# Kernel optimization log

Hardware: AMD Instinct MI355X
Metric: run time of the kernel (lower is better)

The kernel has to match this reference:

```python
import jax, jax.numpy as jnp
import numpy as np

B, T, C = 2, 2048, 2048
H, HD = 16, 128          # n_head, head_dim
DC, DC1 = 672, 672        # kv / q compression dims
DR = 64                   # decoupled rope dim
DN = HD - DR              # nope dim = 64
GATE_CH = 32


def _rope(x, cos, sin):
    # x: (B,T,h,D); cos/sin: (B,T,D//2) -> broadcast over heads
    cos = cos[:, :, None, :]
    sin = sin[:, :, None, :]
    d = x.shape[-1] // 2
    x1, x2 = x[..., :d], x[..., d:]
    return jnp.concatenate([x1 * cos + x2 * sin, -x1 * sin + x2 * cos], axis=-1)


def _rmsnorm(x):
    eps = jnp.finfo(x.dtype).eps
    return x * jax.lax.rsqrt(jnp.mean(jnp.square(x), axis=-1, keepdims=True) + eps)


def setup_inputs() -> dict:
    key = jax.random.key(0)
    ks = jax.random.split(key, 10)
    x = jax.random.normal(ks[0], (B, T, C), jnp.float32)
    ve = jax.random.normal(ks[1], (B, T, H * HD), jnp.float32)
    # rotary tables for d_rope//2 = 32 frequencies
    inv_freq = 1.0 / (10000.0 ** (jnp.arange(DR // 2, dtype=jnp.float32) / (DR // 2)))
    ang = jnp.arange(T, dtype=jnp.float32)[:, None] * inv_freq[None, :]  # (T, DR//2)
    cos = jnp.broadcast_to(jnp.cos(ang)[None], (B, T, DR // 2)).astype(jnp.float32)
    sin = jnp.broadcast_to(jnp.sin(ang)[None], (B, T, DR // 2)).astype(jnp.float32)
    s = 0.02
    w_dkv = s * jax.random.normal(ks[2], (C, DC), jnp.float32)
    w_ukv = s * jax.random.normal(ks[3], (DC, H * (DN + HD)), jnp.float32)
    w_kr = s * jax.random.normal(ks[4], (C, DR), jnp.float32)
    w_dq = s * jax.random.normal(ks[5], (C, DC1), jnp.float32)
    w_q = s * jax.random.normal(ks[6], (DC1, H * HD), jnp.float32)
    w_cproj = s * jax.random.normal(ks[7], (H * HD, C), jnp.float32)
    w_ve_gate = s * jax.random.normal(ks[8], (GATE_CH, H), jnp.float32)
    return {"x": x, "ve": ve, "cos": cos, "sin": sin,
            "w_dkv": w_dkv, "w_ukv": w_ukv, "w_kr": w_kr, "w_dq": w_dq,
            "w_q": w_q, "w_cproj": w_cproj, "w_ve_gate": w_ve_gate,
            "window_size": 0}


def reference(x, ve, cos, sin, w_dkv, w_ukv, w_kr, w_dq, w_q, w_cproj, w_ve_gate, window_size):
    b, t, _ = x.shape
    # low-rank KV path
    c_kv = x @ w_dkv                                   # (B,T,DC)
    kv = (c_kv @ w_ukv).reshape(b, t, H, DN + HD)
    k_nope, v = kv[..., :DN], kv[..., DN:]
    # decoupled rope key (single shared head)
    k_rope = (x @ w_kr).reshape(b, t, 1, DR)
    k_rope = _rope(k_rope, cos, sin)
    # value-embedding gate
    gate = 2.0 * jax.nn.sigmoid(x[..., :GATE_CH] @ w_ve_gate)   # (B,T,H)
    v = v + gate[..., None] * ve.reshape(b, t, H, HD)
    # low-rank Q path
    q = ((x @ w_dq) @ w_q).reshape(b, t, H, HD)
    q_nope, q_rope = q[..., :DN], q[..., DN:]
    q_rope = _rope(q_rope, cos, sin)
    k = jnp.concatenate([k_nope, jnp.broadcast_to(k_rope, (b, t, H, DR))], axis=-1)
    q = jnp.concatenate([q_nope, q_rope], axis=-1)
    q, k = _rmsnorm(q), _rmsnorm(k)
    # causal attention (window_size==0 -> full causal, matching window_size=(-1,-1))
    scale = 1.0 / jnp.sqrt(jnp.float32(HD))
    scores = jnp.einsum('bqhd,bkhd->bhqk', q, k) * scale
    causal = jnp.tril(jnp.ones((t, t), dtype=bool))
    scores = jnp.where(causal[None, None], scores, jnp.finfo(scores.dtype).min)
    att = jax.nn.softmax(scores, axis=-1)
    y = jnp.einsum('bhqk,bkhd->bqhd', att, v).reshape(b, t, H * HD)
    return y @ w_cproj
```

## Files before the change

### kernel.cpp

```cpp
#include <hip/hip_runtime.h>
#include <hip/hip_bf16.h>

typedef unsigned short u16;
typedef unsigned int u32;
typedef __bf16 bf16x8 __attribute__((ext_vector_type(8)));
typedef float f32x4 __attribute__((ext_vector_type(4)));
typedef u16 ushort8 __attribute__((ext_vector_type(8)));

#define TSEQ 2048
#define NHEAD 16

#define GLD16(gp, lp) __builtin_amdgcn_global_load_lds( \
    (__attribute__((address_space(1))) void*)(gp), \
    (__attribute__((address_space(3))) void*)(lp), 16, 0, 0)

static __device__ __forceinline__ float bf2f(u16 u) {
  unsigned int x = ((unsigned int)u) << 16;
  union { unsigned int i; float f; } c; c.i = x; return c.f;
}
static __device__ __forceinline__ u16 f2bf(float f) {
  union { float f; unsigned int i; } c; c.f = f;
  unsigned int x = c.i;
  unsigned int r = (x + 0x7FFFu + ((x >> 16) & 1u)) >> 16;
  return (u16)r;
}
static __device__ __forceinline__ void st_out(u16* p, float v) { *p = f2bf(v); }
static __device__ __forceinline__ void st_out(float* p, float v) { *p = v; }
static __device__ __forceinline__ u32 cvtpk(float lo, float hi) {
  u32 w;
  asm("v_cvt_pk_bf16_f32 %0, %1, %2" : "=v"(w) : "v"(lo), "v"(hi));
  return w;
}

__global__ __launch_bounds__(256) void k_conv_x(const float* __restrict__ x, u16* __restrict__ xb) {
  size_t i = ((size_t)blockIdx.x * 256 + threadIdx.x) * 8;
  float4 a = *(const float4*)(x + i);
  float4 b = *(const float4*)(x + i + 4);
  ushort8 o;
  o[0] = f2bf(a.x); o[1] = f2bf(a.y); o[2] = f2bf(a.z); o[3] = f2bf(a.w);
  o[4] = f2bf(b.x); o[5] = f2bf(b.y); o[6] = f2bf(b.z); o[7] = f2bf(b.w);
  *(ushort8*)(xb + i) = o;
}

__global__ __launch_bounds__(256) void k_tconv(const float* __restrict__ src, u16* __restrict__ dst,
                                               int R, int Cc, int Rpad) {
  __shared__ float sm[32][33];
  int tx = threadIdx.x & 31, ty = threadIdx.x >> 5;
  int r0 = blockIdx.x * 32, c0 = blockIdx.y * 32;
#pragma unroll
  for (int i = 0; i < 4; i++) {
    int r = r0 + ty + 8 * i;
    int c = c0 + tx;
    sm[ty + 8 * i][tx] = (r < R && c < Cc) ? src[(size_t)r * Cc + c] : 0.f;
  }
  __syncthreads();
#pragma unroll
  for (int i = 0; i < 4; i++) {
    int c = c0 + ty + 8 * i;
    dst[(size_t)c * Rpad + r0 + tx] = f2bf(sm[tx][ty + 8 * i]);
  }
}

__global__ __launch_bounds__(256) void k_gate(const float* __restrict__ x, const float* __restrict__ wg,
                                              float* __restrict__ gate) {
  int idx = blockIdx.x * 256 + threadIdx.x;
  int m = idx >> 4, h = idx & 15;
  const float* xr = x + (size_t)m * 2048;
  float s = 0.f;
#pragma unroll
  for (int j = 0; j < 32; j++) s += xr[j] * wg[j * 16 + h];
  gate[idx] = 2.f / (1.f + __expf(-s));
}

template <typename OT>
__global__ __launch_bounds__(256) void k_gemm128(const u16* __restrict__ A, int lda,
                                                 const u16* __restrict__ BT, int ldb,
                                                 OT* __restrict__ C, int ldc,
                                                 int K) {
  __shared__ __align__(16) u16 As[128 * 32];
  __shared__ __align__(16) u16 Bs[128 * 32];
  int t = threadIdx.x;
  int wid = t >> 6, lane = t & 63;
  int m0 = blockIdx.y * 128, n0 = blockIdx.x * 128;
  int c0 = wid * 2;
  int srow0 = c0 * 16 + (lane >> 2);
  int scol = (lane & 3) * 8;
  const u16* Ag0 = A + (size_t)(m0 + srow0) * lda + scol;
  const u16* Ag1 = A + (size_t)(m0 + srow0 + 16) * lda + scol;
  const u16* Bg0 = BT + (size_t)(n0 + srow0) * ldb + scol;
  const u16* Bg1 = BT + (size_t)(n0 + srow0 + 16) * ldb + scol;
  u16* Al0 = &As[c0 * 512];
  u16* Al1 = &As[c0 * 512 + 512];
  u16* Bl0 = &Bs[c0 * 512];
  u16* Bl1 = &Bs[c0 * 512 + 512];
  int wr = (wid >> 1) * 64, wc = (wid & 1) * 64;
  int fr = lane & 15, fo = (lane >> 4) * 8;
  f32x4 acc[4][4];
#pragma unroll
  for (int m = 0; m < 4; m++)
#pragma unroll
    for (int n = 0; n < 4; n++) acc[m][n] = (f32x4){0, 0, 0, 0};
  for (int k0 = 0; k0 < K; k0 += 32) {
    GLD16(Ag0 + k0, Al0);
    GLD16(Ag1 + k0, Al1);
    GLD16(Bg0 + k0, Bl0);
    GLD16(Bg1 + k0, Bl1);
    __syncthreads();
    bf16x8 af[4], bf[4];
#pragma unroll
    for (int m = 0; m < 4; m++) af[m] = *(const bf16x8*)&As[(wr + m * 16 + fr) * 32 + fo];
#pragma unroll
    for (int n = 0; n < 4; n++) bf[n] = *(const bf16x8*)&Bs[(wc + n * 16 + fr) * 32 + fo];
#pragma unroll
    for (int m = 0; m < 4; m++)
#pragma unroll
      for (int n = 0; n < 4; n++)
        acc[m][n] = __builtin_amdgcn_mfma_f32_16x16x32_bf16(af[m], bf[n], acc[m][n], 0, 0, 0);
    __syncthreads();
  }
  int cr = (lane >> 4) * 4, cc = lane & 15;
#pragma unroll
  for (int m = 0; m < 4; m++)
#pragma unroll
    for (int n = 0; n < 4; n++)
#pragma unroll
      for (int r = 0; r < 4; r++)
        st_out(&C[(size_t)(m0 + wr + m * 16 + cr + r) * ldc + n0 + wc + n * 16 + cc], acc[m][n][r]);
}

__global__ __launch_bounds__(256) void k_gemm_dual(const u16* __restrict__ catout,
                                                   const u16* __restrict__ wukvT,
                                                   u16* __restrict__ kvb,
                                                   const u16* __restrict__ wqT,
                                                   const float* __restrict__ cosp,
                                                   const float* __restrict__ sinp,
                                                   u16* __restrict__ qf) {
  __shared__ __align__(16) u16 As[128 * 32];
  __shared__ __align__(16) u16 Bs[128 * 32];
  int t = threadIdx.x;
  int wid = t >> 6, lane = t & 63;
  int bx = blockIdx.x;
  bool isq = (bx >= 24);
  int nx = isq ? bx - 24 : bx;
  int m0 = blockIdx.y * 128, n0 = nx * 128;
  const u16* A = isq ? catout + 768 : catout;
  const u16* BT = isq ? wqT : wukvT;
  int c0 = wid * 2;
  int srow0 = c0 * 16 + (lane >> 2);
  int scol = (lane & 3) * 8;
  const u16* Ag0 = A + (size_t)(m0 + srow0) * 1664 + scol;
  const u16* Ag1 = A + (size_t)(m0 + srow0 + 16) * 1664 + scol;
  const u16* Bg0 = BT + (size_t)(n0 + srow0) * 768 + scol;
  const u16* Bg1 = BT + (size_t)(n0 + srow0 + 16) * 768 + scol;
  u16* Al0 = &As[c0 * 512];
  u16* Al1 = &As[c0 * 512 + 512];
  u16* Bl0 = &Bs[c0 * 512];
  u16* Bl1 = &Bs[c0 * 512 + 512];
  int wr = (wid >> 1) * 64, wc = (wid & 1) * 64;
  int fr = lane & 15, fo = (lane >> 4) * 8;
  f32x4 acc[4][4];
#pragma unroll
  for (int m = 0; m < 4; m++)
#pragma unroll
    for (int n = 0; n < 4; n++) acc[m][n] = (f32x4){0, 0, 0, 0};
  for (int k0 = 0; k0 < 768; k0 += 32) {
    GLD16(Ag0 + k0, Al0);
    GLD16(Ag1 + k0, Al1);
    GLD16(Bg0 + k0, Bl0);
    GLD16(Bg1 + k0, Bl1);
    __syncthreads();
    bf16x8 af[4], bf[4];
#pragma unroll
    for (int m = 0; m < 4; m++) af[m] = *(const bf16x8*)&As[(wr + m * 16 + fr) * 32 + fo];
#pragma unroll
    for (int n = 0; n < 4; n++) bf[n] = *(const bf16x8*)&Bs[(wc + n * 16 + fr) * 32 + fo];
#pragma unroll
    for (int m = 0; m < 4; m++)
#pragma unroll
      for (int n = 0; n < 4; n++)
        acc[m][n] = __builtin_amdgcn_mfma_f32_16x16x32_bf16(af[m], bf[n], acc[m][n], 0, 0, 0);
    __syncthreads();
  }
  int cr = (lane >> 4) * 4, cc = lane & 15;
  if (!isq) {
#pragma unroll
    for (int m = 0; m < 4; m++)
#pragma unroll
      for (int n = 0; n < 4; n++)
#pragma unroll
        for (int r = 0; r < 4; r++)
          kvb[(size_t)(m0 + wr + m * 16 + cr + r) * 3072 + n0 + wc + n * 16 + cc] = f2bf(acc[m][n][r]);
    return;
  }
  int h = nx;
  int wch = wid & 1;
  int wrg = wid >> 1;
  if (wch == 1) {
#pragma unroll
    for (int m = 0; m < 4; m++)
#pragma unroll
      for (int r = 0; r < 4; r++) {
        int grow = m0 + wr + m * 16 + cr + r;
#pragma unroll
        for (int n = 0; n < 2; n++) {
          int i = n * 16 + cc;
          float cth = cosp[(size_t)grow * 32 + i];
          float sth = sinp[(size_t)grow * 32 + i];
          float x1 = acc[m][n][r], x2 = acc[m][n + 2][r];
          acc[m][n][r]     = x1 * cth + x2 * sth;
          acc[m][n + 2][r] = x2 * cth - x1 * sth;
        }
      }
  }
  float part[4][4];
#pragma unroll
  for (int m = 0; m < 4; m++)
#pragma unroll
    for (int r = 0; r < 4; r++) {
      float s2 = 0.f;
#pragma unroll
      for (int n = 0; n < 4; n++) s2 += acc[m][n][r] * acc[m][n][r];
#pragma unroll
      for (int o = 1; o < 16; o <<= 1) s2 += __shfl_xor(s2, o, 64);
      part[m][r] = s2;
    }
  float* xs = (float*)As;
  if (cc == 0) {
#pragma unroll
    for (int m = 0; m < 4; m++)
#pragma unroll
      for (int r = 0; r < 4; r++)
        xs[(wrg * 2 + wch) * 64 + m * 16 + cr + r] = part[m][r];
  }
  __syncthreads();
#pragma unroll
  for (int m = 0; m < 4; m++)
#pragma unroll
    for (int r = 0; r < 4; r++) {
      int lrow = m * 16 + cr + r;
      float tot = part[m][r] + xs[(wrg * 2 + (wch ^ 1)) * 64 + lrow];
      float rms = rsqrtf(tot * (1.f / 128.f) + 1.1920929e-7f) * 0.1275174245f;
      int grow = m0 + wr + lrow;
      int b2 = grow >> 11, tt = grow & 2047;
      size_t base = (((size_t)(b2 * NHEAD + h)) * TSEQ + tt) * 128 + wch * 64;
#pragma unroll
      for (int n = 0; n < 4; n++)
        qf[base + n * 16 + cc] = f2bf(acc[m][n][r] * rms);
    }
}

__global__ __launch_bounds__(256) void k_build_k(const u16* __restrict__ kv, const u16* __restrict__ kr,
                                                 const float* __restrict__ cosp, const float* __restrict__ sinp,
                                                 u16* __restrict__ ksw) {
  __shared__ __align__(16) u16 sm[8192];
  int tid = threadIdx.x, wid = tid >> 6, lane = tid & 63;
  int bh = blockIdx.x >> 5, tile = blockIdx.x & 31;
  int b = bh >> 4, h = bh & 15;
  int d0 = lane * 2;
  for (int rr = 0; rr < 16; rr++) {
    int row = wid * 16 + rr;
    int t = tile * 64 + row;
    int m = b * TSEQ + t;
    float v[2];
#pragma unroll
    for (int e = 0; e < 2; e++) {
      int d = d0 + e;
      float val;
      if (d < 64) {
        val = bf2f(kv[(size_t)m * 3072 + h * 192 + d]);
      } else {
        int dd = d - 64, i = dd & 31;
        float c = cosp[m * 32 + i], s = sinp[m * 32 + i];
        float x1 = bf2f(kr[(size_t)m * 1664 + i]), x2 = bf2f(kr[(size_t)m * 1664 + 32 + i]);
        val = (dd < 32) ? (x1 * c + x2 * s) : (x2 * c - x1 * s);
      }
      v[e] = val;
    }
    float ss = v[0] * v[0] + v[1] * v[1];
#pragma unroll
    for (int o = 1; o < 64; o <<= 1) ss += __shfl_xor(ss, o, 64);
    float rms = rsqrtf(ss * (1.f / 128.f) + 1.1920929e-7f);
    int a = (row * 256 + d0 * 2) ^ ((row & 7) << 4);
    sm[a >> 1] = f2bf(v[0] * rms);
    sm[(a >> 1) + 1] = f2bf(v[1] * rms);
  }
  __syncthreads();
  u16* dst = ksw + ((size_t)(bh * 32 + tile)) * 8192 + tid * 32;
  const u16* src = sm + tid * 32;
#pragma unroll
  for (int j = 0; j < 4; j++)
    *(ushort8*)(dst + j * 8) = *(const ushort8*)(src + j * 8);
}

__global__ __launch_bounds__(256) void k_build_v(const u16* __restrict__ kv, const float* __restrict__ ve,
                                                 const float* __restrict__ gate, u16* __restrict__ vsw) {
  __shared__ __align__(16) char sm[128 * 128];
  int bh = blockIdx.x >> 5, tile = blockIdx.x & 31;
  int t0 = tile * 64;
  int b = bh >> 4, h = bh & 15;
  int tt = threadIdx.x >> 2, dp = (threadIdx.x & 3) * 32;
  int m = b * TSEQ + t0 + tt;
  float g = gate[m * 16 + h];
  const u16* kvp = kv + (size_t)m * 3072 + h * 192 + 64 + dp;
  const float* vep = ve + (size_t)m * 2048 + h * 128 + dp;
  ushort8 kvv[4];
  float4 vev[8];
#pragma unroll
  for (int u = 0; u < 4; u++) kvv[u] = *(const ushort8*)(kvp + u * 8);
#pragma unroll
  for (int u = 0; u < 8; u++) vev[u] = *(const float4*)(vep + u * 4);
#pragma unroll
  for (int j = 0; j < 32; j++) {
    float vvf = ((const float*)&vev[j >> 2])[j & 3];
    float v = bf2f(kvv[j >> 3][j & 7]) + g * vvf;
    int row = dp + j;
    int a = row * 128 + tt * 2;
    *(u16*)(sm + (a ^ ((row & 7) << 4))) = f2bf(v);
  }
  __syncthreads();
  u16* dst = vsw + ((size_t)(bh * 32 + tile)) * 8192 + threadIdx.x * 32;
  const u16* src = (const u16*)sm + threadIdx.x * 32;
#pragma unroll
  for (int j = 0; j < 4; j++)
    *(ushort8*)(dst + j * 8) = *(const ushort8*)(src + j * 8);
}

__global__ __launch_bounds__(256, 2) void k_attn(const u16* __restrict__ qf, const u16* __restrict__ ksw,
                                                 const u16* __restrict__ vsw, u16* __restrict__ y) {
  __shared__ __align__(16) u16 kvbuf[2][2][8192];
  __shared__ __align__(16) char plds_all[4][4096];
  int tid = threadIdx.x, wid = tid >> 6, lane = tid & 63;
  int gq = lane >> 4, c = lane & 15;
  int task = (blockIdx.x & 7) * 64 + (blockIdx.x >> 3);
  int bh = task >> 4;
  int tq = task & 15;
  int qb = ((task >> 5) & 1) ? tq : 15 - tq;
  int nt = 2 * qb + 2;
  int q0w = qb * 128 + wid * 32;
  const u16* qp = qf + (size_t)bh * TSEQ * 128;
  const u16* kswb = ksw + (size_t)bh * 32 * 8192;
  const u16* vswb = vsw + (size_t)bh * 32 * 8192;
  char* plds = plds_all[wid];
  int swz = (c & 7) << 4;
  bf16x8 qfr[2][4];
#pragma unroll
  for (int rg = 0; rg < 2; rg++)
#pragma unroll
    for (int kc = 0; kc < 4; kc++)
      qfr[rg][kc] = *(const bf16x8*)(qp + (size_t)(q0w + rg * 16 + c) * 128 + kc * 32 + gq * 8);
  f32x4 oacc[2][8];
#pragma unroll
  for (int rg = 0; rg < 2; rg++)
#pragma unroll
    for (int nd = 0; nd < 8; nd++) oacc[rg][nd] = (f32x4){0, 0, 0, 0};
  float mreg[2] = {-1e30f, -1e30f}, lreg[2] = {0.f, 0.f};
  int chunk = wid * 4;
#pragma unroll
  for (int j = 0; j < 4; j++) {
    GLD16(kswb + (chunk + j) * 512 + lane * 8, &kvbuf[0][0][(chunk + j) * 512]);
    GLD16(vswb + (chunk + j) * 512 + lane * 8, &kvbuf[0][1][(chunk + j) * 512]);
  }
  __syncthreads();
  for (int it = 0; it < nt; it++) {
    int cur = it & 1;
    if (it + 1 < nt) {
      const u16* kt = kswb + (size_t)(it + 1) * 8192;
      const u16* vt = vswb + (size_t)(it + 1) * 8192;
#pragma unroll
      for (int j = 0; j < 4; j++) {
        GLD16(kt + (chunk + j) * 512 + lane * 8, &kvbuf[cur ^ 1][0][(chunk + j) * 512]);
        GLD16(vt + (chunk + j) * 512 + lane * 8, &kvbuf[cur ^ 1][1][(chunk + j) * 512]);
      }
    }
    int kt0 = it * 64;
    if (kt0 <= q0w + 31) {
      const char* Kt = (const char*)kvbuf[cur][0];
      const char* Vt = (const char*)kvbuf[cur][1];
      bool maskit = (kt0 + 63 > q0w);
      f32x4 sacc[2][4];
#pragma unroll
      for (int rg = 0; rg < 2; rg++)
#pragma unroll
        for (int s = 0; s < 4; s++) sacc[rg][s] = (f32x4){0, 0, 0, 0};
#pragma unroll
      for (int s = 0; s < 4; s++) {
        int row = s * 16 + c;
#pragma unroll
        for (int kc = 0; kc < 4; kc++) {
          int a = (row * 256 + (kc * 32 + gq * 8) * 2) ^ ((row & 7) << 4);
          bf16x8 kfr = *(const bf16x8*)(Kt + a);
          sacc[0][s] = __builtin_amdgcn_mfma_f32_16x16x32_bf16(kfr, qfr[0][kc], sacc[0][s], 0, 0, 0);
          sacc[1][s] = __builtin_amdgcn_mfma_f32_16x16x32_bf16(kfr, qfr[1][kc], sacc[1][s], 0, 0, 0);
        }
      }
      if (maskit) {
#pragma unroll
        for (int rg = 0; rg < 2; rg++) {
          int qrow = q0w + rg * 16 + c;
#pragma unroll
          for (int s = 0; s < 4; s++)
#pragma unroll
            for (int r = 0; r < 4; r++) {
              int key = kt0 + s * 16 + gq * 4 + r;
              sacc[rg][s][r] = (key <= qrow) ? sacc[rg][s][r] : -3e38f;
            }
        }
      }
      float mx[2];
#pragma unroll
      for (int rg = 0; rg < 2; rg++) {
        float m2 = sacc[rg][0][0];
#pragma unroll
        for (int s = 0; s < 4; s++)
#pragma unroll
          for (int r = 0; r < 4; r++) m2 = fmaxf(m2, sacc[rg][s][r]);
        m2 = fmaxf(m2, __shfl_xor(m2, 16, 64));
        m2 = fmaxf(m2, __shfl_xor(m2, 32, 64));
        mx[rg] = m2;
      }
      bool ok = (mx[0] - mreg[0] <= 11.f) && (mx[1] - mreg[1] <= 11.f);
      if (!__all(ok)) {
#pragma unroll
        for (int rg = 0; rg < 2; rg++) {
          float mn = fmaxf(mreg[rg], mx[rg]);
          float fac = exp2f(mreg[rg] - mn);
          lreg[rg] *= fac;
          float fq[4];
#pragma unroll
          for (int r = 0; r < 4; r++) fq[r] = __shfl(fac, gq * 4 + r, 64);
#pragma unroll
          for (int nd = 0; nd < 8; nd++)
#pragma unroll
            for (int r = 0; r < 4; r++) oacc[rg][nd][r] *= fq[r];
          mreg[rg] = mn;
        }
      }
#pragma unroll
      for (int rg = 0; rg < 2; rg++) {
        float p[4][4];
        float rs = 0.f;
#pragma unroll
        for (int s = 0; s < 4; s++)
#pragma unroll
          for (int r = 0; r < 4; r++) {
            p[s][r] = exp2f(sacc[rg][s][r] - mreg[rg]);
            rs += p[s][r];
          }
        rs += __shfl_xor(rs, 16, 64);
        rs += __shfl_xor(rs, 32, 64);
        lreg[rg] += rs;
#pragma unroll
        for (int s = 0; s < 4; s++) {
          u32 w0 = cvtpk(p[s][0], p[s][1]);
          u32 w1 = cvtpk(p[s][2], p[s][3]);
          int a = (rg * 2048 + c * 128 + s * 32 + gq * 8) ^ swz;
          *(uint2*)(plds + a) = make_uint2(w0, w1);
        }
      }
#pragma unroll
      for (int kc2 = 0; kc2 < 2; kc2++) {
        int a0 = (c * 128 + kc2 * 64 + gq * 16) ^ swz;
        bf16x8 pa0 = *(const bf16x8*)(plds + a0);
        bf16x8 pa1 = *(const bf16x8*)(plds + 2048 + a0);
#pragma unroll
        for (int nd = 0; nd < 8; nd++) {
          int vrow = nd * 16 + c;
          int av = (vrow * 128 + (kc2 * 32 + gq * 8) * 2) ^ ((vrow & 7) << 4);
          bf16x8 vfr = *(const bf16x8*)(Vt + av);
          oacc[0][nd] = __builtin_amdgcn_mfma_f32_16x16x32_bf16(pa0, vfr, oacc[0][nd], 0, 0, 0);
          oacc[1][nd] = __builtin_amdgcn_mfma_f32_16x16x32_bf16(pa1, vfr, oacc[1][nd], 0, 0, 0);
        }
      }
    }
    __syncthreads();
  }
  int b2 = bh >> 4, h2 = bh & 15;
#pragma unroll
  for (int rg = 0; rg < 2; rg++) {
    float linv = 1.f / lreg[rg];
    float inv[4];
#pragma unroll
    for (int r = 0; r < 4; r++) inv[r] = __shfl(linv, gq * 4 + r, 64);
#pragma unroll
    for (int nd = 0; nd < 8; nd++) {
#pragma unroll
      for (int r = 0; r < 4; r++) {
        size_t offo = ((size_t)(b2 * TSEQ + q0w + rg * 16 + gq * 4 + r)) * 2048 + h2 * 128 + nd * 16 + c;
        y[offo] = f2bf(oacc[rg][nd][r] * inv[r]);
      }
    }
  }
}

extern "C" void kernel_launch(void* const* d_in, const int* in_sizes, int n_in,
                              void* d_out, int out_size, void* d_ws, size_t ws_size,
                              hipStream_t stream) {
  (void)in_sizes; (void)n_in; (void)out_size; (void)ws_size;
  const float* x      = (const float*)d_in[0];
  const float* ve     = (const float*)d_in[1];
  const float* cosp   = (const float*)d_in[2];
  const float* sinp   = (const float*)d_in[3];
  const float* w_dkv  = (const float*)d_in[4];
  const float* w_ukv  = (const float*)d_in[5];
  const float* w_kr   = (const float*)d_in[6];
  const float* w_dq   = (const float*)d_in[7];
  const float* w_q    = (const float*)d_in[8];
  const float* w_cp   = (const float*)d_in[9];
  const float* w_vg   = (const float*)d_in[10];
  float* out = (float*)d_out;

  char* ws = (char*)d_ws;
  size_t off = 0;
  auto alloc = [&](size_t bytes) -> char* {
    char* p = ws + off;
    off += (bytes + 255) & ~(size_t)255;
    return p;
  };
  u16* xb     = (u16*)alloc(4096ull * 2048 * 2);
  u16* wcatT  = (u16*)alloc(1664ull * 2048 * 2);
  u16* wukvT  = (u16*)alloc(3072ull * 768 * 2);
  u16* wqT    = (u16*)alloc(2048ull * 768 * 2);
  u16* wcpT   = (u16*)alloc(2048ull * 2048 * 2);
  u16* catout = (u16*)alloc(4096ull * 1664 * 2);
  u16* kvb    = (u16*)alloc(4096ull * 3072 * 2);
  float* gateb = (float*)alloc(4096ull * 16 * 4);
  u16* qfb    = (u16*)alloc(2ull * 16 * 2048 * 128 * 2);
  u16* kswb   = (u16*)alloc(32ull * 32 * 8192 * 2);
  u16* vswb   = (u16*)alloc(32ull * 32 * 8192 * 2);
  u16* yb = xb;

  k_conv_x<<<dim3(4096), dim3(256), 0, stream>>>(x, xb);
  k_tconv<<<dim3(64, 24), dim3(256), 0, stream>>>(w_dkv, wcatT,               2048, 672, 2048);
  k_tconv<<<dim3(64, 24), dim3(256), 0, stream>>>(w_dq,  wcatT + 768 * 2048,  2048, 672, 2048);
  k_tconv<<<dim3(64, 2),  dim3(256), 0, stream>>>(w_kr,  wcatT + 1536 * 2048, 2048, 64, 2048);
  k_tconv<<<dim3(24, 96), dim3(256), 0, stream>>>(w_ukv, wukvT, 672, 3072, 768);
  k_tconv<<<dim3(24, 64), dim3(256), 0, stream>>>(w_q,   wqT,   672, 2048, 768);
  k_tconv<<<dim3(64, 64), dim3(256), 0, stream>>>(w_cp,  wcpT,  2048, 2048, 2048);
  k_gate<<<dim3(256), dim3(256), 0, stream>>>(x, w_vg, gateb);

  k_gemm128<u16><<<dim3(13, 32), dim3(256), 0, stream>>>(xb, 2048, wcatT, 2048, catout, 1664, 2048);
  k_gemm_dual<<<dim3(40, 32), dim3(256), 0, stream>>>(catout, wukvT, kvb, wqT, cosp, sinp, qfb);

  k_build_k<<<dim3(1024), dim3(256), 0, stream>>>(kvb, catout + 1536, cosp, sinp, kswb);
  k_build_v<<<dim3(1024), dim3(256), 0, stream>>>(kvb, ve, gateb, vswb);

  k_attn<<<dim3(512), dim3(256), 0, stream>>>(qfb, kswb, vswb, yb);

  k_gemm128<float><<<dim3(16, 32), dim3(256), 0, stream>>>(yb, 2048, wcpT, 2048, out, 2048, 2048);
}
```

Baseline: 339.4 us.

## Shrink attention blocks, read V directly from global in transposed layout, merge weight transposes

The attention kernel now uses 2-wave blocks over 64-row query tiles with 1024 blocks and higher occupancy. Only K is double-buffered in LDS; V is written by k_build_v as a plain transposed (d, t) array and read straight from global/L2 in the PV MFMA loop. This removes the causal-skip branch, since each wave always covers the whole tile range. The six weight-transpose launches are merged into one kernel to cut launch overhead. The direct V global loads trade LDS traffic and space for possibly higher load latency inside the MFMA loop.

```diff
diff --git a/kernel.cpp b/kernel.cpp
--- a/kernel.cpp
+++ b/kernel.cpp
@@ -42,11 +42,22 @@
   *(ushort8*)(xb + i) = o;
 }
 
-__global__ __launch_bounds__(256) void k_tconv(const float* __restrict__ src, u16* __restrict__ dst,
-                                               int R, int Cc, int Rpad) {
+__global__ __launch_bounds__(256) void k_tconv_all(const float* __restrict__ w_dkv, const float* __restrict__ w_dq,
+                                                   const float* __restrict__ w_kr, const float* __restrict__ w_ukv,
+                                                   const float* __restrict__ w_q, const float* __restrict__ w_cp,
+                                                   u16* __restrict__ wcatT, u16* __restrict__ wukvT,
+                                                   u16* __restrict__ wqT, u16* __restrict__ wcpT) {
   __shared__ float sm[32][33];
+  int z = blockIdx.x;
+  const float* src; u16* dst; int R, Cc, Rpad, bx, by;
+  if (z < 1536)       { src = w_dkv; dst = wcatT;              R = 2048; Cc = 672;  Rpad = 2048; int l = z;        bx = l % 64; by = l / 64; }
+  else if (z < 3072)  { src = w_dq;  dst = wcatT + 768 * 2048; R = 2048; Cc = 672;  Rpad = 2048; int l = z - 1536; bx = l % 64; by = l / 64; }
+  else if (z < 3200)  { src = w_kr;  dst = wcatT + 1536 * 2048;R = 2048; Cc = 64;   Rpad = 2048; int l = z - 3072; bx = l % 64; by = l / 64; }
+  else if (z < 5504)  { src = w_ukv; dst = wukvT;              R = 672;  Cc = 3072; Rpad = 768;  int l = z - 3200; bx = l % 24; by = l / 24; }
+  else if (z < 7040)  { src = w_q;   dst = wqT;                R = 672;  Cc = 2048; Rpad = 768;  int l = z - 5504; bx = l % 24; by = l / 24; }
+  else                { src = w_cp;  dst = wcpT;               R = 2048; Cc = 2048; Rpad = 2048; int l = z - 7040; bx = l % 64; by = l / 64; }
   int tx = threadIdx.x & 31, ty = threadIdx.x >> 5;
-  int r0 = blockIdx.x * 32, c0 = blockIdx.y * 32;
+  int r0 = bx * 32, c0 = by * 32;
 #pragma unroll
   for (int i = 0; i < 4; i++) {
     int r = r0 + ty + 8 * i;
@@ -293,10 +304,9 @@
 }
 
 __global__ __launch_bounds__(256) void k_build_v(const u16* __restrict__ kv, const float* __restrict__ ve,
-                                                 const float* __restrict__ gate, u16* __restrict__ vsw) {
+                                                 const float* __restrict__ gate, u16* __restrict__ vt) {
   __shared__ __align__(16) char sm[128 * 128];
-  int bh = blockIdx.x >> 5, tile = blockIdx.x & 31;
-  int t0 = tile * 64;
+  int bh = blockIdx.x >> 5, t0 = (blockIdx.x & 31) * 64;
   int b = bh >> 4, h = bh & 15;
   int tt = threadIdx.x >> 2, dp = (threadIdx.x & 3) * 32;
   int m = b * TSEQ + t0 + tt;
@@ -318,28 +328,30 @@
     *(u16*)(sm + (a ^ ((row & 7) << 4))) = f2bf(v);
   }
   __syncthreads();
-  u16* dst = vsw + ((size_t)(bh * 32 + tile)) * 8192 + threadIdx.x * 32;
-  const u16* src = (const u16*)sm + threadIdx.x * 32;
-#pragma unroll
-  for (int j = 0; j < 4; j++)
-    *(ushort8*)(dst + j * 8) = *(const ushort8*)(src + j * 8);
-}
-
-__global__ __launch_bounds__(256, 2) void k_attn(const u16* __restrict__ qf, const u16* __restrict__ ksw,
-                                                 const u16* __restrict__ vsw, u16* __restrict__ y) {
-  __shared__ __align__(16) u16 kvbuf[2][2][8192];
-  __shared__ __align__(16) char plds_all[4][4096];
+  int d = threadIdx.x >> 1, tp = (threadIdx.x & 1) * 32;
+  u16* dst = vt + ((size_t)bh * 128 + d) * TSEQ + t0 + tp;
+#pragma unroll
+  for (int j = 0; j < 32; j += 8) {
+    int a = d * 128 + (tp + j) * 2;
+    *(ushort8*)(dst + j) = *(const ushort8*)(sm + (a ^ ((d & 7) << 4)));
+  }
+}
+
+__global__ __launch_bounds__(128, 4) void k_attn(const u16* __restrict__ qf, const u16* __restrict__ ksw,
+                                                 const u16* __restrict__ vt, u16* __restrict__ y) {
+  __shared__ __align__(16) u16 kbuf[2][8192];
+  __shared__ __align__(16) char plds_all[2][4096];
   int tid = threadIdx.x, wid = tid >> 6, lane = tid & 63;
   int gq = lane >> 4, c = lane & 15;
-  int task = (blockIdx.x & 7) * 64 + (blockIdx.x >> 3);
-  int bh = task >> 4;
-  int tq = task & 15;
-  int qb = ((task >> 5) & 1) ? tq : 15 - tq;
-  int nt = 2 * qb + 2;
-  int q0w = qb * 128 + wid * 32;
+  int task = (blockIdx.x & 7) * 128 + (blockIdx.x >> 3);
+  int bh = task >> 5;
+  int tq = task & 31;
+  int qb = (tq & 1) ? (tq >> 1) : (31 - (tq >> 1));
+  int nt = qb + 1;
+  int q0w = qb * 64 + wid * 32;
   const u16* qp = qf + (size_t)bh * TSEQ * 128;
   const u16* kswb = ksw + (size_t)bh * 32 * 8192;
-  const u16* vswb = vsw + (size_t)bh * 32 * 8192;
+  const u16* vp = vt + (size_t)bh * 128 * TSEQ;
   char* plds = plds_all[wid];
   int swz = (c & 7) << 4;
   bf16x8 qfr[2][4];
@@ -354,122 +366,112 @@
 #pragma unroll
     for (int nd = 0; nd < 8; nd++) oacc[rg][nd] = (f32x4){0, 0, 0, 0};
   float mreg[2] = {-1e30f, -1e30f}, lreg[2] = {0.f, 0.f};
-  int chunk = wid * 4;
-#pragma unroll
-  for (int j = 0; j < 4; j++) {
-    GLD16(kswb + (chunk + j) * 512 + lane * 8, &kvbuf[0][0][(chunk + j) * 512]);
-    GLD16(vswb + (chunk + j) * 512 + lane * 8, &kvbuf[0][1][(chunk + j) * 512]);
-  }
+  int chunk = wid * 8;
+#pragma unroll
+  for (int j = 0; j < 8; j++)
+    GLD16(kswb + (chunk + j) * 512 + lane * 8, &kbuf[0][(chunk + j) * 512]);
   __syncthreads();
   for (int it = 0; it < nt; it++) {
     int cur = it & 1;
     if (it + 1 < nt) {
       const u16* kt = kswb + (size_t)(it + 1) * 8192;
-      const u16* vt = vswb + (size_t)(it + 1) * 8192;
-#pragma unroll
-      for (int j = 0; j < 4; j++) {
-        GLD16(kt + (chunk + j) * 512 + lane * 8, &kvbuf[cur ^ 1][0][(chunk + j) * 512]);
-        GLD16(vt + (chunk + j) * 512 + lane * 8, &kvbuf[cur ^ 1][1][(chunk + j) * 512]);
-      }
+#pragma unroll
+      for (int j = 0; j < 8; j++)
+        GLD16(kt + (chunk + j) * 512 + lane * 8, &kbuf[cur ^ 1][(chunk + j) * 512]);
     }
     int kt0 = it * 64;
-    if (kt0 <= q0w + 31) {
-      const char* Kt = (const char*)kvbuf[cur][0];
-      const char* Vt = (const char*)kvbuf[cur][1];
-      bool maskit = (kt0 + 63 > q0w);
-      f32x4 sacc[2][4];
-#pragma unroll
-      for (int rg = 0; rg < 2; rg++)
-#pragma unroll
-        for (int s = 0; s < 4; s++) sacc[rg][s] = (f32x4){0, 0, 0, 0};
+    const char* Kt = (const char*)kbuf[cur];
+    bool maskit = (kt0 + 63 > q0w);
+    f32x4 sacc[2][4];
+#pragma unroll
+    for (int rg = 0; rg < 2; rg++)
+#pragma unroll
+      for (int s = 0; s < 4; s++) sacc[rg][s] = (f32x4){0, 0, 0, 0};
+#pragma unroll
+    for (int s = 0; s < 4; s++) {
+      int row = s * 16 + c;
+#pragma unroll
+      for (int kc = 0; kc < 4; kc++) {
+        int a = (row * 256 + (kc * 32 + gq * 8) * 2) ^ ((row & 7) << 4);
+        bf16x8 kfr = *(const bf16x8*)(Kt + a);
+        sacc[0][s] = __builtin_amdgcn_mfma_f32_16x16x32_bf16(kfr, qfr[0][kc], sacc[0][s], 0, 0, 0);
+        sacc[1][s] = __builtin_amdgcn_mfma_f32_16x16x32_bf16(kfr, qfr[1][kc], sacc[1][s], 0, 0, 0);
+      }
+    }
+    if (maskit) {
+#pragma unroll
+      for (int rg = 0; rg < 2; rg++) {
+        int qrow = q0w + rg * 16 + c;
+#pragma unroll
+        for (int s = 0; s < 4; s++)
+#pragma unroll
+          for (int r = 0; r < 4; r++) {
+            int key = kt0 + s * 16 + gq * 4 + r;
+            sacc[rg][s][r] = (key <= qrow) ? sacc[rg][s][r] : -3e38f;
+          }
+      }
+    }
+    float mx[2];
+#pragma unroll
+    for (int rg = 0; rg < 2; rg++) {
+      float m2 = sacc[rg][0][0];
+#pragma unroll
+      for (int s = 0; s < 4; s++)
+#pragma unroll
+        for (int r = 0; r < 4; r++) m2 = fmaxf(m2, sacc[rg][s][r]);
+      m2 = fmaxf(m2, __shfl_xor(m2, 16, 64));
+      m2 = fmaxf(m2, __shfl_xor(m2, 32, 64));
+      mx[rg] = m2;
+    }
+    bool ok = (mx[0] - mreg[0] <= 11.f) && (mx[1] - mreg[1] <= 11.f);
+    if (!__all(ok)) {
+#pragma unroll
+      for (int rg = 0; rg < 2; rg++) {
+        float mn = fmaxf(mreg[rg], mx[rg]);
+        float fac = exp2f(mreg[rg] - mn);
+        lreg[rg] *= fac;
+        float fq[4];
+#pragma unroll
+        for (int r = 0; r < 4; r++) fq[r] = __shfl(fac, gq * 4 + r, 64);
+#pragma unroll
+        for (int nd = 0; nd < 8; nd++)
+#pragma unroll
+          for (int r = 0; r < 4; r++) oacc[rg][nd][r] *= fq[r];
+        mreg[rg] = mn;
+      }
+    }
+#pragma unroll
+    for (int rg = 0; rg < 2; rg++) {
+      float p[4][4];
+      float rs = 0.f;
+#pragma unroll
+      for (int s = 0; s < 4; s++)
+#pragma unroll
+        for (int r = 0; r < 4; r++) {
+          p[s][r] = exp2f(sacc[rg][s][r] - mreg[rg]);
+          rs += p[s][r];
+        }
+      rs += __shfl_xor(rs, 16, 64);
+      rs += __shfl_xor(rs, 32, 64);
+      lreg[rg] += rs;
 #pragma unroll
       for (int s = 0; s < 4; s++) {
-        int row = s * 16 + c;
-#pragma unroll
-        for (int kc = 0; kc < 4; kc++) {
-          int a = (row * 256 + (kc * 32 + gq * 8) * 2) ^ ((row & 7) << 4);
-          bf16x8 kfr = *(const bf16x8*)(Kt + a);
-          sacc[0][s] = __builtin_amdgcn_mfma_f32_16x16x32_bf16(kfr, qfr[0][kc], sacc[0][s], 0, 0, 0);
-          sacc[1][s] = __builtin_amdgcn_mfma_f32_16x16x32_bf16(kfr, qfr[1][kc], sacc[1][s], 0, 0, 0);
-        }
-      }
-      if (maskit) {
-#pragma unroll
-        for (int rg = 0; rg < 2; rg++) {
-          int qrow = q0w + rg * 16 + c;
-#pragma unroll
-          for (int s = 0; s < 4; s++)
-#pragma unroll
-            for (int r = 0; r < 4; r++) {
-              int key = kt0 + s * 16 + gq * 4 + r;
-              sacc[rg][s][r] = (key <= qrow) ? sacc[rg][s][r] : -3e38f;
-            }
-        }
-      }
-      float mx[2];
-#pragma unroll
-      for (int rg = 0; rg < 2; rg++) {
-        float m2 = sacc[rg][0][0];
-#pragma unroll
-        for (int s = 0; s < 4; s++)
-#pragma unroll
-          for (int r = 0; r < 4; r++) m2 = fmaxf(m2, sacc[rg][s][r]);
-        m2 = fmaxf(m2, __shfl_xor(m2, 16, 64));
-        m2 = fmaxf(m2, __shfl_xor(m2, 32, 64));
-        mx[rg] = m2;
-      }
-      bool ok = (mx[0] - mreg[0] <= 11.f) && (mx[1] - mreg[1] <= 11.f);
-      if (!__all(ok)) {
-#pragma unroll
-        for (int rg = 0; rg < 2; rg++) {
-          float mn = fmaxf(mreg[rg], mx[rg]);
-          float fac = exp2f(mreg[rg] - mn);
-          lreg[rg] *= fac;
-          float fq[4];
-#pragma unroll
-          for (int r = 0; r < 4; r++) fq[r] = __shfl(fac, gq * 4 + r, 64);
-#pragma unroll
-          for (int nd = 0; nd < 8; nd++)
-#pragma unroll
-            for (int r = 0; r < 4; r++) oacc[rg][nd][r] *= fq[r];
-          mreg[rg] = mn;
-        }
-      }
-#pragma unroll
-      for (int rg = 0; rg < 2; rg++) {
-        float p[4][4];
-        float rs = 0.f;
-#pragma unroll
-        for (int s = 0; s < 4; s++)
-#pragma unroll
-          for (int r = 0; r < 4; r++) {
-            p[s][r] = exp2f(sacc[rg][s][r] - mreg[rg]);
-            rs += p[s][r];
-          }
-        rs += __shfl_xor(rs, 16, 64);
-        rs += __shfl_xor(rs, 32, 64);
-        lreg[rg] += rs;
-#pragma unroll
-        for (int s = 0; s < 4; s++) {
-          u32 w0 = cvtpk(p[s][0], p[s][1]);
-          u32 w1 = cvtpk(p[s][2], p[s][3]);
-          int a = (rg * 2048 + c * 128 + s * 32 + gq * 8) ^ swz;
-          *(uint2*)(plds + a) = make_uint2(w0, w1);
-        }
-      }
-#pragma unroll
-      for (int kc2 = 0; kc2 < 2; kc2++) {
-        int a0 = (c * 128 + kc2 * 64 + gq * 16) ^ swz;
-        bf16x8 pa0 = *(const bf16x8*)(plds + a0);
-        bf16x8 pa1 = *(const bf16x8*)(plds + 2048 + a0);
-#pragma unroll
-        for (int nd = 0; nd < 8; nd++) {
-          int vrow = nd * 16 + c;
-          int av = (vrow * 128 + (kc2 * 32 + gq * 8) * 2) ^ ((vrow & 7) << 4);
-          bf16x8 vfr = *(const bf16x8*)(Vt + av);
-          oacc[0][nd] = __builtin_amdgcn_mfma_f32_16x16x32_bf16(pa0, vfr, oacc[0][nd], 0, 0, 0);
-          oacc[1][nd] = __builtin_amdgcn_mfma_f32_16x16x32_bf16(pa1, vfr, oacc[1][nd], 0, 0, 0);
-        }
+        u32 w0 = cvtpk(p[s][0], p[s][1]);
+        u32 w1 = cvtpk(p[s][2], p[s][3]);
+        int a = (rg * 2048 + c * 128 + s * 32 + gq * 8) ^ swz;
+        *(uint2*)(plds + a) = make_uint2(w0, w1);
+      }
+    }
+#pragma unroll
+    for (int kc2 = 0; kc2 < 2; kc2++) {
+      int a0 = (c * 128 + kc2 * 64 + gq * 16) ^ swz;
+      bf16x8 pa0 = *(const bf16x8*)(plds + a0);
+      bf16x8 pa1 = *(const bf16x8*)(plds + 2048 + a0);
+#pragma unroll
+      for (int nd = 0; nd < 8; nd++) {
+        bf16x8 vfr = *(const bf16x8*)(vp + (size_t)(nd * 16 + c) * TSEQ + kt0 + kc2 * 32 + gq * 8);
+        oacc[0][nd] = __builtin_amdgcn_mfma_f32_16x16x32_bf16(pa0, vfr, oacc[0][nd], 0, 0, 0);
+        oacc[1][nd] = __builtin_amdgcn_mfma_f32_16x16x32_bf16(pa1, vfr, oacc[1][nd], 0, 0, 0);
       }
     }
     __syncthreads();
@@ -526,25 +528,21 @@
   float* gateb = (float*)alloc(4096ull * 16 * 4);
   u16* qfb    = (u16*)alloc(2ull * 16 * 2048 * 128 * 2);
   u16* kswb   = (u16*)alloc(32ull * 32 * 8192 * 2);
-  u16* vswb   = (u16*)alloc(32ull * 32 * 8192 * 2);
+  u16* vtb    = (u16*)alloc(32ull * 128 * 2048 * 2);
   u16* yb = xb;
 
   k_conv_x<<<dim3(4096), dim3(256), 0, stream>>>(x, xb);
-  k_tconv<<<dim3(64, 24), dim3(256), 0, stream>>>(w_dkv, wcatT,               2048, 672, 2048);
-  k_tconv<<<dim3(64, 24), dim3(256), 0, stream>>>(w_dq,  wcatT + 768 * 2048,  2048, 672, 2048);
-  k_tconv<<<dim3(64, 2),  dim3(256), 0, stream>>>(w_kr,  wcatT + 1536 * 2048, 2048, 64, 2048);
-  k_tconv<<<dim3(24, 96), dim3(256), 0, stream>>>(w_ukv, wukvT, 672, 3072, 768);
-  k_tconv<<<dim3(24, 64), dim3(256), 0, stream>>>(w_q,   wqT,   672, 2048, 768);
-  k_tconv<<<dim3(64, 64), dim3(256), 0, stream>>>(w_cp,  wcpT,  2048, 2048, 2048);
+  k_tconv_all<<<dim3(11136), dim3(256), 0, stream>>>(w_dkv, w_dq, w_kr, w_ukv, w_q, w_cp,
+                                                     wcatT, wukvT, wqT, wcpT);
   k_gate<<<dim3(256), dim3(256), 0, stream>>>(x, w_vg, gateb);
 
   k_gemm128<u16><<<dim3(13, 32), dim3(256), 0, stream>>>(xb, 2048, wcatT, 2048, catout, 1664, 2048);
   k_gemm_dual<<<dim3(40, 32), dim3(256), 0, stream>>>(catout, wukvT, kvb, wqT, cosp, sinp, qfb);
 
   k_build_k<<<dim3(1024), dim3(256), 0, stream>>>(kvb, catout + 1536, cosp, sinp, kswb);
-  k_build_v<<<dim3(1024), dim3(256), 0, stream>>>(kvb, ve, gateb, vswb);
-
-  k_attn<<<dim3(512), dim3(256), 0, stream>>>(qfb, kswb, vswb, yb);
+  k_build_v<<<dim3(1024), dim3(256), 0, stream>>>(kvb, ve, gateb, vtb);
+
+  k_attn<<<dim3(1024), dim3(128), 0, stream>>>(qfb, kswb, vtb, yb);
 
   k_gemm128<float><<<dim3(16, 32), dim3(256), 0, stream>>>(yb, 2048, wcpT, 2048, out, 2048, 2048);
 }
```

Result: slower. 507.5 us (+49.5%).
